# Kernel optimization log

Measured on AMD Instinct MI355X. Metric: run time of the kernel, lower is better.

The kernel has to match this reference:

```python
import jax, jax.numpy as jnp
import numpy as np

N_NODES = 50000
BN_EPS = 1e-5


def setup_inputs() -> dict:
    key = jax.random.key(0)
    ks = jax.random.split(key, 6)
    N, E, CIN, CH, COUT = N_NODES, 800000, 128, 256, 128
    node_feat = jax.random.normal(ks[0], (N, CIN), dtype=jnp.float32)
    edge_index = jax.random.randint(ks[1], (2, E), 0, N, dtype=jnp.int64)
    # Glorot-ish init for weights
    W1 = jax.random.normal(ks[2], (CIN, CH), dtype=jnp.float32) / np.sqrt(CIN)
    b1 = jnp.zeros((CH,), dtype=jnp.float32)
    bn_gamma = jnp.ones((CH,), dtype=jnp.float32)
    bn_beta = jnp.zeros((CH,), dtype=jnp.float32)
    W2 = jax.random.normal(ks[3], (CH, COUT), dtype=jnp.float32) / np.sqrt(CH)
    b2 = jnp.zeros((COUT,), dtype=jnp.float32)
    return {"node_feat": node_feat, "edge_index": edge_index, "W1": W1, "b1": b1,
            "bn_gamma": bn_gamma, "bn_beta": bn_beta, "W2": W2, "b2": b2}


def gcn_conv(x, W, b, src, dst, n_nodes):
    """PyG GCNConv: out = D^-1/2 (A+I) D^-1/2 (x W) + b."""
    h = x @ W                                   # [N, C_out]
    loop = jnp.arange(n_nodes, dtype=src.dtype)
    src_f = jnp.concatenate([src, loop])        # self-loops appended
    dst_f = jnp.concatenate([dst, loop])
    deg = jax.ops.segment_sum(jnp.ones_like(dst_f, dtype=h.dtype), dst_f,
                              num_segments=n_nodes)
    dinv = jax.lax.rsqrt(jnp.maximum(deg, 1.0))  # deg >= 1 due to self-loops
    norm = dinv[src_f] * dinv[dst_f]             # [E+N]
    msg = h[src_f] * norm[:, None]               # gather + scale
    return jax.ops.segment_sum(msg, dst_f, num_segments=n_nodes) + b


def batch_norm(x, gamma, beta):
    mean = jnp.mean(x, axis=0)
    var = jnp.mean((x - mean) ** 2, axis=0)      # biased var (torch BN normalization)
    return (x - mean) * jax.lax.rsqrt(var + BN_EPS) * gamma + beta


def reference(node_feat, edge_index, W1, b1, bn_gamma, bn_beta, W2, b2):
    src, dst = edge_index[0], edge_index[1]
    x = gcn_conv(node_feat, W1, b1, src, dst, N_NODES)
    x = batch_norm(x, bn_gamma, bn_beta)
    x = jax.nn.relu(x)
    # dropout is identity at inference
    x = gcn_conv(x, W2, b2, src, dst, N_NODES)
    return x
```

## Files before the change

### kernel.cpp

```cpp
#include <hip/hip_runtime.h>
#include <hip/hip_fp16.h>

#define CIN 128
#define CH 256
#define COUT 128
#define BN_EPS 1e-5f

typedef __attribute__((ext_vector_type(8))) short bf16x8;
typedef __attribute__((ext_vector_type(4))) float f32x4;

__device__ __forceinline__ short f2bf(float x) {
    unsigned u = __float_as_uint(x);
    unsigned r = (u + 0x7fffu + ((u >> 16) & 1u)) >> 16;
    return (short)r;
}
__device__ __forceinline__ float bf2f(short h) {
    return __uint_as_float(((unsigned)(unsigned short)h) << 16);
}

__global__ void k_deg(const int* __restrict__ dst, int* __restrict__ degi,
                      unsigned short* __restrict__ rank, int E) {
    int e = blockIdx.x * 256 + threadIdx.x;
    if (e < E) rank[e] = (unsigned short)atomicAdd(&degi[dst[e]], 1);
}

__global__ void k_scan1(const int* __restrict__ degi, float* __restrict__ dinv,
                        int* __restrict__ blocksum, int N) {
    __shared__ int s[256];
    int i = blockIdx.x * 256 + threadIdx.x;
    int v = (i < N) ? degi[i] : 0;
    if (i < N) dinv[i] = rsqrtf((float)(v + 1));
    s[threadIdx.x] = v;
    __syncthreads();
    for (int st = 128; st > 0; st >>= 1) {
        if (threadIdx.x < st) s[threadIdx.x] += s[threadIdx.x + st];
        __syncthreads();
    }
    if (threadIdx.x == 0) blocksum[blockIdx.x] = s[0];
}

__global__ void k_scan3(const int* __restrict__ degi, const int* __restrict__ blocksum,
                        int nb, int* __restrict__ rowstart, int N, int E) {
    __shared__ int sb[256];
    __shared__ int s[256];
    int bv = (threadIdx.x < nb) ? blocksum[threadIdx.x] : 0;
    sb[threadIdx.x] = bv;
    __syncthreads();
    for (int st = 1; st < 256; st <<= 1) {
        int t = (threadIdx.x >= st) ? sb[threadIdx.x - st] : 0;
        __syncthreads();
        sb[threadIdx.x] += t;
        __syncthreads();
    }
    int boff = (blockIdx.x == 0) ? 0 : sb[blockIdx.x - 1];

    int i = blockIdx.x * 256 + threadIdx.x;
    int v = (i < N) ? degi[i] : 0;
    s[threadIdx.x] = v;
    __syncthreads();
    for (int st = 1; st < 256; st <<= 1) {
        int t = (threadIdx.x >= st) ? s[threadIdx.x - st] : 0;
        __syncthreads();
        s[threadIdx.x] += t;
        __syncthreads();
    }
    if (i < N) rowstart[i] = s[threadIdx.x] - v + boff;
    if (blockIdx.x == 0 && threadIdx.x == 0) rowstart[N] = E;
}

__global__ void k_fill(const int* __restrict__ src, const int* __restrict__ dst,
                       const unsigned short* __restrict__ rank,
                       const int* __restrict__ rowstart,
                       unsigned short* __restrict__ csr, int E) {
    int e = blockIdx.x * 256 + threadIdx.x;
    if (e >= E) return;
    int d = dst[e];
    int pos = rowstart[d] + (int)rank[e];
    __builtin_nontemporal_store((unsigned short)src[e], &csr[pos]);
}

__global__ void k_prep(const float* __restrict__ W1, const float* __restrict__ W2,
                       short* __restrict__ W1Th, short* __restrict__ W1Tl,
                       short* __restrict__ W2Th, short* __restrict__ W2Tl,
                       const float4* __restrict__ nf, short4* __restrict__ nfb, int n4) {
    int t = blockIdx.x * 256 + threadIdx.x;
    if (t < 32768) {
        int n = t >> 7, k = t & 127;
        float v = W1[k * 256 + n];
        short h = f2bf(v);
        W1Th[t] = h;
        W1Tl[t] = f2bf(v - bf2f(h));
    } else if (t < 65536) {
        int u = t - 32768;
        int n = u >> 8, k = u & 255;
        float v = W2[k * 128 + n];
        short h = f2bf(v);
        W2Th[u] = h;
        W2Tl[u] = f2bf(v - bf2f(h));
    } else {
        int u = t - 65536;
        if (u < n4) {
            float4 v = nf[u];
            short4 s;
            s.x = f2bf(v.x); s.y = f2bf(v.y); s.z = f2bf(v.z); s.w = f2bf(v.w);
            nfb[u] = s;
        }
    }
}

template <int MODE>
__global__ __launch_bounds__(256) void k_gather(const short* __restrict__ xb,
                                                const int* __restrict__ rowstart,
                                                const unsigned short* __restrict__ csr,
                                                const float* __restrict__ dinv,
                                                const float* __restrict__ bias,
                                                float* __restrict__ out,
                                                short* __restrict__ ob, int N) {
    int t = blockIdx.x * 256 + threadIdx.x;
    int r = t >> 4;
    int c = t & 15;
    if (r >= N) return;
    float di = dinv[r];
    float w0 = di * di;
    bf16x8 sv = *(const bf16x8*)(xb + (size_t)r * 128 + c * 8);
    float acc[8];
    #pragma unroll
    for (int j = 0; j < 8; ++j) acc[j] = bf2f(sv[j]) * w0;
    int e0 = rowstart[r], e1 = rowstart[r + 1];
    int e = e0;
    for (; e + 7 < e1; e += 8) {
        int s[8];
        #pragma unroll
        for (int i = 0; i < 8; ++i) s[i] = csr[e + i];
        float w[8];
        #pragma unroll
        for (int i = 0; i < 8; ++i) w[i] = dinv[s[i]] * di;
        bf16x8 x[8];
        #pragma unroll
        for (int i = 0; i < 8; ++i) x[i] = *(const bf16x8*)(xb + (size_t)s[i] * 128 + c * 8);
        #pragma unroll
        for (int i = 0; i < 8; ++i)
            #pragma unroll
            for (int j = 0; j < 8; ++j) acc[j] = fmaf(w[i], bf2f(x[i][j]), acc[j]);
    }
    for (; e + 3 < e1; e += 4) {
        int s[4];
        #pragma unroll
        for (int i = 0; i < 4; ++i) s[i] = csr[e + i];
        float w[4];
        #pragma unroll
        for (int i = 0; i < 4; ++i) w[i] = dinv[s[i]] * di;
        bf16x8 x[4];
        #pragma unroll
        for (int i = 0; i < 4; ++i) x[i] = *(const bf16x8*)(xb + (size_t)s[i] * 128 + c * 8);
        #pragma unroll
        for (int i = 0; i < 4; ++i)
            #pragma unroll
            for (int j = 0; j < 8; ++j) acc[j] = fmaf(w[i], bf2f(x[i][j]), acc[j]);
    }
    for (; e < e1; ++e) {
        int s0 = csr[e];
        float ww = dinv[s0] * di;
        bf16x8 x0 = *(const bf16x8*)(xb + (size_t)s0 * 128 + c * 8);
        #pragma unroll
        for (int j = 0; j < 8; ++j) acc[j] = fmaf(ww, bf2f(x0[j]), acc[j]);
    }
    if (MODE == 0) {
        bf16x8 h;
        #pragma unroll
        for (int j = 0; j < 8; ++j) h[j] = f2bf(acc[j]);
        *(bf16x8*)(ob + (size_t)r * 128 + c * 8) = h;
    } else {
        float4 b0 = *(const float4*)(bias + c * 8);
        float4 b1 = *(const float4*)(bias + c * 8 + 4);
        float4 o0 = make_float4(acc[0] + b0.x, acc[1] + b0.y, acc[2] + b0.z, acc[3] + b0.w);
        float4 o1 = make_float4(acc[4] + b1.x, acc[5] + b1.y, acc[6] + b1.z, acc[7] + b1.w);
        *(float4*)(out + (size_t)r * 128 + c * 8) = o0;
        *(float4*)(out + (size_t)r * 128 + c * 8 + 4) = o1;
    }
}

__device__ __forceinline__ bf16x8 bnrelu8(bf16x8 raw, const float* __restrict__ scsh, int c) {
    float4 sc0 = *(const float4*)(scsh + c);
    float4 sc1 = *(const float4*)(scsh + c + 4);
    float4 sh0 = *(const float4*)(scsh + 256 + c);
    float4 sh1 = *(const float4*)(scsh + 256 + c + 4);
    bf16x8 o;
    o[0] = f2bf(fmaxf(fmaf(bf2f(raw[0]), sc0.x, sh0.x), 0.f));
    o[1] = f2bf(fmaxf(fmaf(bf2f(raw[1]), sc0.y, sh0.y), 0.f));
    o[2] = f2bf(fmaxf(fmaf(bf2f(raw[2]), sc0.z, sh0.z), 0.f));
    o[3] = f2bf(fmaxf(fmaf(bf2f(raw[3]), sc0.w, sh0.w), 0.f));
    o[4] = f2bf(fmaxf(fmaf(bf2f(raw[4]), sc1.x, sh1.x), 0.f));
    o[5] = f2bf(fmaxf(fmaf(bf2f(raw[5]), sc1.y, sh1.y), 0.f));
    o[6] = f2bf(fmaxf(fmaf(bf2f(raw[6]), sc1.z, sh1.z), 0.f));
    o[7] = f2bf(fmaxf(fmaf(bf2f(raw[7]), sc1.w, sh1.w), 0.f));
    return o;
}

template <int K, int NOUT, bool STATS, bool BIAS, bool BNRELU>
__global__ __launch_bounds__(256, 2) void k_gemm(const short* __restrict__ A,
                                                 const short* __restrict__ Bh,
                                                 const short* __restrict__ Bl,
                                                 const float* __restrict__ bias,
                                                 const float* __restrict__ scsh,
                                                 short* __restrict__ C,
                                                 float* __restrict__ stats, int M) {
    constexpr int CT = NOUT / 64;
    constexpr int KS = K / 32;
    constexpr int LROW = NOUT + 8;
    __shared__ short lds[64 * LROW];
    int wave = threadIdx.x >> 6;
    int lane = threadIdx.x & 63;
    int m = lane & 15;
    int q = lane >> 4;
    int row0 = blockIdx.x * 64;
    int colw = wave * (NOUT / 4);

    bf16x8 bhf[CT][KS], blf[CT][KS];
    #pragma unroll
    for (int ct = 0; ct < CT; ++ct) {
        #pragma unroll
        for (int ks = 0; ks < KS; ++ks) {
            size_t bo = (size_t)(colw + ct * 16 + m) * K + ks * 32 + q * 8;
            bhf[ct][ks] = *(const bf16x8*)(Bh + bo);
            blf[ct][ks] = *(const bf16x8*)(Bl + bo);
        }
    }

    const short* pa[4];
    #pragma unroll
    for (int rt = 0; rt < 4; ++rt) {
        int ar = row0 + rt * 16 + m;
        if (ar >= M) ar = M - 1;
        pa[rt] = A + (size_t)ar * K + q * 8;
    }

    f32x4 acc[4][CT];
    #pragma unroll
    for (int rt = 0; rt < 4; ++rt)
        #pragma unroll
        for (int ct = 0; ct < CT; ++ct)
            acc[rt][ct] = (f32x4){0.f, 0.f, 0.f, 0.f};

    #pragma unroll
    for (int ks = 0; ks < KS; ++ks) {
        bf16x8 af[4];
        #pragma unroll
        for (int rt = 0; rt < 4; ++rt) {
            bf16x8 raw = *(const bf16x8*)(pa[rt] + ks * 32);
            af[rt] = BNRELU ? bnrelu8(raw, scsh, ks * 32 + q * 8) : raw;
        }
        #pragma unroll
        for (int ct = 0; ct < CT; ++ct) {
            #pragma unroll
            for (int rt = 0; rt < 4; ++rt) {
                acc[rt][ct] = __builtin_amdgcn_mfma_f32_16x16x32_bf16(af[rt], bhf[ct][ks], acc[rt][ct], 0, 0, 0);
                acc[rt][ct] = __builtin_amdgcn_mfma_f32_16x16x32_bf16(af[rt], blf[ct][ks], acc[rt][ct], 0, 0, 0);
            }
        }
    }

    #pragma unroll
    for (int ct = 0; ct < CT; ++ct) {
        int col = colw + ct * 16 + m;
        float bv = BIAS ? bias[col] : 0.f;
        float s = 0.f, sq = 0.f;
        #pragma unroll
        for (int rt = 0; rt < 4; ++rt) {
            #pragma unroll
            for (int r = 0; r < 4; ++r) {
                int lrow = rt * 16 + q * 4 + r;
                float v = acc[rt][ct][r] + bv;
                if (STATS && row0 + lrow < M) { s += v; sq = fmaf(v, v, sq); }
                lds[lrow * LROW + col] = f2bf(v);
            }
        }
        if (STATS) {
            s += __shfl_xor(s, 16, 64);
            s += __shfl_xor(s, 32, 64);
            sq += __shfl_xor(sq, 16, 64);
            sq += __shfl_xor(sq, 32, 64);
            if (lane < 16) {
                unsafeAtomicAdd(&stats[col], s);
                unsafeAtomicAdd(&stats[256 + col], sq);
            }
        }
    }
    __syncthreads();
    constexpr int CPR = NOUT / 8;
    constexpr int TOT = 64 * CPR;
    #pragma unroll
    for (int i = 0; i < TOT / 256; ++i) {
        int idx = i * 256 + threadIdx.x;
        int row = idx / CPR;
        int ch = idx % CPR;
        if (row0 + row < M)
            *(bf16x8*)(C + (size_t)(row0 + row) * NOUT + ch * 8) =
                *(const bf16x8*)(lds + row * LROW + ch * 8);
    }
}

__global__ void k_bnfinal(const float* __restrict__ stats, const float* __restrict__ gamma,
                          const float* __restrict__ beta, float* __restrict__ scsh, int N) {
    int c = threadIdx.x;
    float invN = 1.0f / (float)N;
    float mean = stats[c] * invN;
    float var = stats[256 + c] * invN - mean * mean;
    var = fmaxf(var, 0.f);
    float inv = rsqrtf(var + BN_EPS);
    float sc = gamma[c] * inv;
    scsh[c] = sc;
    scsh[256 + c] = fmaf(-mean, sc, beta[c]);
}

extern "C" void kernel_launch(void* const* d_in, const int* in_sizes, int n_in,
                              void* d_out, int out_size, void* d_ws, size_t ws_size,
                              hipStream_t stream) {
    const float* nf    = (const float*)d_in[0];
    const int*   ei    = (const int*)d_in[1];
    const float* W1    = (const float*)d_in[2];
    const float* b1    = (const float*)d_in[3];
    const float* gamma = (const float*)d_in[4];
    const float* beta  = (const float*)d_in[5];
    const float* W2    = (const float*)d_in[6];
    const float* b2    = (const float*)d_in[7];
    float* out = (float*)d_out;

    const int N = in_sizes[0] / CIN;
    const int E = in_sizes[1] / 2;
    const int* src = ei;
    const int* dst = ei + E;

    char* ws = (char*)d_ws;
    auto align256 = [](size_t x) { return (x + 255) & ~(size_t)255; };
    size_t off = 0;
    int*   degi = (int*)(ws + off);      off += align256((size_t)N * 4);
    float* stats = (float*)(ws + off);   off += align256(512 * 4);
    size_t zspan = off;
    float* dinv = (float*)(ws + off);    off += align256((size_t)N * 4);
    int*   rowstart = (int*)(ws + off);  off += align256((size_t)(N + 1) * 4);
    int*   blocksum = (int*)(ws + off);  off += align256(256 * 4);
    float* scsh = (float*)(ws + off);    off += align256(512 * 4);
    short* W1Th = (short*)(ws + off);    off += align256(32768 * 2);
    short* W1Tl = (short*)(ws + off);    off += align256(32768 * 2);
    short* W2Th = (short*)(ws + off);    off += align256(32768 * 2);
    short* W2Tl = (short*)(ws + off);    off += align256(32768 * 2);
    unsigned short* rank = (unsigned short*)(ws + off); off += align256((size_t)E * 2);
    unsigned short* csr = (unsigned short*)(ws + off);  off += align256((size_t)E * 2);
    short* nfb = (short*)(ws + off);     off += align256((size_t)N * CIN * 2);
    short* agg1b = (short*)(ws + off);   off += align256((size_t)N * CIN * 2);
    short* x1b = (short*)(ws + off);     off += align256((size_t)N * CH * 2);
    short* yb = (short*)(ws + off);      off += align256((size_t)N * COUT * 2);

    int nbN = (N + 255) / 256;
    int nbE = (E + 255) / 256;
    int n4 = N * 32;

    hipMemsetAsync(ws, 0, zspan, stream);

    k_prep<<<(65536 + n4 + 255) / 256, 256, 0, stream>>>(
        W1, W2, W1Th, W1Tl, W2Th, W2Tl, (const float4*)nf, (short4*)nfb, n4);

    k_deg<<<nbE, 256, 0, stream>>>(dst, degi, rank, E);
    k_scan1<<<nbN, 256, 0, stream>>>(degi, dinv, blocksum, N);
    k_scan3<<<nbN, 256, 0, stream>>>(degi, blocksum, nbN, rowstart, N, E);
    k_fill<<<nbE, 256, 0, stream>>>(src, dst, rank, rowstart, csr, E);

    k_gather<0><<<(N * 16 + 255) / 256, 256, 0, stream>>>(
        nfb, rowstart, csr, dinv, nullptr, nullptr, agg1b, N);

    k_gemm<CIN, CH, true, true, false><<<(N + 63) / 64, 256, 0, stream>>>(
        agg1b, W1Th, W1Tl, b1, nullptr, x1b, stats, N);

    k_bnfinal<<<1, 256, 0, stream>>>(stats, gamma, beta, scsh, N);

    k_gemm<CH, COUT, false, false, true><<<(N + 63) / 64, 256, 0, stream>>>(
        x1b, W2Th, W2Tl, nullptr, scsh, yb, nullptr, N);

    k_gather<1><<<(N * 16 + 255) / 256, 256, 0, stream>>>(
        yb, rowstart, csr, dinv, b2, out, nullptr, N);
}
```

Baseline: 299.9 us.

## Stage A tile in LDS and stream pre-swizzled weights per k-step in GEMMs

The GEMM kernels no longer keep the whole hi/lo bf16 weight fragment set in registers. Weights are pre-swizzled in the prep kernel into an MFMA-fragment-contiguous layout so each lane loads its fragments with one coalesced 16-byte read per k-step. The A tile is loaded cooperatively into padded LDS, with BN+ReLU applied once per element, instead of strided per-lane global loads. This cuts register pressure and uncoalesced A reads, but adds weight loads inside the k-loop and an extra LDS round trip plus barriers.

```diff
diff --git a/kernel.cpp b/kernel.cpp
--- a/kernel.cpp
+++ b/kernel.cpp
@@ -80,23 +80,30 @@
 }
 
 __global__ void k_prep(const float* __restrict__ W1, const float* __restrict__ W2,
-                       short* __restrict__ W1Th, short* __restrict__ W1Tl,
-                       short* __restrict__ W2Th, short* __restrict__ W2Tl,
+                       short* __restrict__ W1sw, short* __restrict__ W2sw,
                        const float4* __restrict__ nf, short4* __restrict__ nfb, int n4) {
     int t = blockIdx.x * 256 + threadIdx.x;
     if (t < 32768) {
-        int n = t >> 7, k = t & 127;
-        float v = W1[k * 256 + n];
+        int n = t >> 7, kk = t & 127;
+        float v = W1[kk * 256 + n];
         short h = f2bf(v);
-        W1Th[t] = h;
-        W1Tl[t] = f2bf(v - bf2f(h));
+        short l = f2bf(v - bf2f(h));
+        int t16 = n >> 4, m = n & 15;
+        int ks = kk >> 5, q = (kk >> 3) & 3, j = kk & 7;
+        int idx = (t16 * 4 + ks) * 1024 + (q * 16 + m) * 8 + j;
+        W1sw[idx] = h;
+        W1sw[idx + 512] = l;
     } else if (t < 65536) {
         int u = t - 32768;
-        int n = u >> 8, k = u & 255;
-        float v = W2[k * 128 + n];
+        int n = u >> 8, kk = u & 255;
+        float v = W2[kk * 128 + n];
         short h = f2bf(v);
-        W2Th[u] = h;
-        W2Tl[u] = f2bf(v - bf2f(h));
+        short l = f2bf(v - bf2f(h));
+        int t16 = n >> 4, m = n & 15;
+        int ks = kk >> 5, q = (kk >> 3) & 3, j = kk & 7;
+        int idx = (t16 * 8 + ks) * 1024 + (q * 16 + m) * 8 + j;
+        W2sw[idx] = h;
+        W2sw[idx + 512] = l;
     } else {
         int u = t - 65536;
         if (u < n4) {
@@ -199,41 +206,36 @@
 
 template <int K, int NOUT, bool STATS, bool BIAS, bool BNRELU>
 __global__ __launch_bounds__(256, 2) void k_gemm(const short* __restrict__ A,
-                                                 const short* __restrict__ Bh,
-                                                 const short* __restrict__ Bl,
+                                                 const short* __restrict__ Bsw,
                                                  const float* __restrict__ bias,
                                                  const float* __restrict__ scsh,
                                                  short* __restrict__ C,
                                                  float* __restrict__ stats, int M) {
     constexpr int CT = NOUT / 64;
     constexpr int KS = K / 32;
+    constexpr int KP = K + 8;
     constexpr int LROW = NOUT + 8;
-    __shared__ short lds[64 * LROW];
-    int wave = threadIdx.x >> 6;
-    int lane = threadIdx.x & 63;
+    constexpr int LSZ = (64 * KP > 64 * LROW) ? 64 * KP : 64 * LROW;
+    __shared__ __align__(16) short lds[LSZ];
+    int tid = threadIdx.x;
+    int wave = tid >> 6;
+    int lane = tid & 63;
     int m = lane & 15;
     int q = lane >> 4;
     int row0 = blockIdx.x * 64;
-    int colw = wave * (NOUT / 4);
-
-    bf16x8 bhf[CT][KS], blf[CT][KS];
-    #pragma unroll
-    for (int ct = 0; ct < CT; ++ct) {
-        #pragma unroll
-        for (int ks = 0; ks < KS; ++ks) {
-            size_t bo = (size_t)(colw + ct * 16 + m) * K + ks * 32 + q * 8;
-            bhf[ct][ks] = *(const bf16x8*)(Bh + bo);
-            blf[ct][ks] = *(const bf16x8*)(Bl + bo);
-        }
-    }
-
-    const short* pa[4];
-    #pragma unroll
-    for (int rt = 0; rt < 4; ++rt) {
-        int ar = row0 + rt * 16 + m;
-        if (ar >= M) ar = M - 1;
-        pa[rt] = A + (size_t)ar * K + q * 8;
-    }
+
+    constexpr int CPRA = K / 8;
+    #pragma unroll
+    for (int i = 0; i < (64 * CPRA) / 256; ++i) {
+        int idx = i * 256 + tid;
+        int r = idx / CPRA, cc = idx % CPRA;
+        int gr = row0 + r;
+        if (gr >= M) gr = M - 1;
+        bf16x8 v = *(const bf16x8*)(A + (size_t)gr * K + cc * 8);
+        if (BNRELU) v = bnrelu8(v, scsh, cc * 8);
+        *(bf16x8*)(lds + r * KP + cc * 8) = v;
+    }
+    __syncthreads();
 
     f32x4 acc[4][CT];
     #pragma unroll
@@ -244,25 +246,30 @@
 
     #pragma unroll
     for (int ks = 0; ks < KS; ++ks) {
+        bf16x8 bh[CT], bl[CT];
+        #pragma unroll
+        for (int ct = 0; ct < CT; ++ct) {
+            const short* bp = Bsw + (size_t)((wave * CT + ct) * KS + ks) * 1024 + lane * 8;
+            bh[ct] = *(const bf16x8*)bp;
+            bl[ct] = *(const bf16x8*)(bp + 512);
+        }
         bf16x8 af[4];
         #pragma unroll
-        for (int rt = 0; rt < 4; ++rt) {
-            bf16x8 raw = *(const bf16x8*)(pa[rt] + ks * 32);
-            af[rt] = BNRELU ? bnrelu8(raw, scsh, ks * 32 + q * 8) : raw;
-        }
-        #pragma unroll
-        for (int ct = 0; ct < CT; ++ct) {
+        for (int rt = 0; rt < 4; ++rt)
+            af[rt] = *(const bf16x8*)(lds + (rt * 16 + m) * KP + ks * 32 + q * 8);
+        #pragma unroll
+        for (int ct = 0; ct < CT; ++ct)
             #pragma unroll
             for (int rt = 0; rt < 4; ++rt) {
-                acc[rt][ct] = __builtin_amdgcn_mfma_f32_16x16x32_bf16(af[rt], bhf[ct][ks], acc[rt][ct], 0, 0, 0);
-                acc[rt][ct] = __builtin_amdgcn_mfma_f32_16x16x32_bf16(af[rt], blf[ct][ks], acc[rt][ct], 0, 0, 0);
+                acc[rt][ct] = __builtin_amdgcn_mfma_f32_16x16x32_bf16(af[rt], bh[ct], acc[rt][ct], 0, 0, 0);
+                acc[rt][ct] = __builtin_amdgcn_mfma_f32_16x16x32_bf16(af[rt], bl[ct], acc[rt][ct], 0, 0, 0);
             }
-        }
-    }
+    }
+    __syncthreads();
 
     #pragma unroll
     for (int ct = 0; ct < CT; ++ct) {
-        int col = colw + ct * 16 + m;
+        int col = wave * (NOUT / 4) + ct * 16 + m;
         float bv = BIAS ? bias[col] : 0.f;
         float s = 0.f, sq = 0.f;
         #pragma unroll
@@ -288,10 +295,9 @@
     }
     __syncthreads();
     constexpr int CPR = NOUT / 8;
-    constexpr int TOT = 64 * CPR;
-    #pragma unroll
-    for (int i = 0; i < TOT / 256; ++i) {
-        int idx = i * 256 + threadIdx.x;
+    #pragma unroll
+    for (int i = 0; i < (64 * CPR) / 256; ++i) {
+        int idx = i * 256 + tid;
         int row = idx / CPR;
         int ch = idx % CPR;
         if (row0 + row < M)
@@ -341,10 +347,8 @@
     int*   rowstart = (int*)(ws + off);  off += align256((size_t)(N + 1) * 4);
     int*   blocksum = (int*)(ws + off);  off += align256(256 * 4);
     float* scsh = (float*)(ws + off);    off += align256(512 * 4);
-    short* W1Th = (short*)(ws + off);    off += align256(32768 * 2);
-    short* W1Tl = (short*)(ws + off);    off += align256(32768 * 2);
-    short* W2Th = (short*)(ws + off);    off += align256(32768 * 2);
-    short* W2Tl = (short*)(ws + off);    off += align256(32768 * 2);
+    short* W1sw = (short*)(ws + off);    off += align256(65536 * 2);
+    short* W2sw = (short*)(ws + off);    off += align256(65536 * 2);
     unsigned short* rank = (unsigned short*)(ws + off); off += align256((size_t)E * 2);
     unsigned short* csr = (unsigned short*)(ws + off);  off += align256((size_t)E * 2);
     short* nfb = (short*)(ws + off);     off += align256((size_t)N * CIN * 2);
@@ -359,7 +363,7 @@
     hipMemsetAsync(ws, 0, zspan, stream);
 
     k_prep<<<(65536 + n4 + 255) / 256, 256, 0, stream>>>(
-        W1, W2, W1Th, W1Tl, W2Th, W2Tl, (const float4*)nf, (short4*)nfb, n4);
+        W1, W2, W1sw, W2sw, (const float4*)nf, (short4*)nfb, n4);
 
     k_deg<<<nbE, 256, 0, stream>>>(dst, degi, rank, E);
     k_scan1<<<nbN, 256, 0, stream>>>(degi, dinv, blocksum, N);
@@ -370,12 +374,12 @@
         nfb, rowstart, csr, dinv, nullptr, nullptr, agg1b, N);
 
     k_gemm<CIN, CH, true, true, false><<<(N + 63) / 64, 256, 0, stream>>>(
-        agg1b, W1Th, W1Tl, b1, nullptr, x1b, stats, N);
+        agg1b, W1sw, b1, nullptr, x1b, stats, N);
 
     k_bnfinal<<<1, 256, 0, stream>>>(stats, gamma, beta, scsh, N);
 
     k_gemm<CH, COUT, false, false, true><<<(N + 63) / 64, 256, 0, stream>>>(
-        x1b, W2Th, W2Tl, nullptr, scsh, yb, nullptr, N);
+        x1b, W2sw, nullptr, scsh, yb, nullptr, N);
 
     k_gather<1><<<(N * 16 + 255) / 256, 256, 0, stream>>>(
         yb, rowstart, csr, dinv, b2, out, nullptr, N);
```

Result: faster. 276.9 us (-7.7%).
